# Kernel optimization log

Measured on AMD Instinct MI355X. Metric: run time of the kernel, lower is better.

The kernel has to match this reference:

```python
import jax, jax.numpy as jnp
import numpy as np

B, S, D, H, L = 4, 2048, 256, 4, 2
DK = D // H
V, T = 32000, 1000


def setup_inputs() -> dict:
    key = jax.random.key(0)
    ks = jax.random.split(key, 20)
    sc = 0.02
    event_emb = jax.random.normal(ks[0], (V, D), jnp.float32) * sc
    event_emb = event_emb.at[0].set(0.0)  # padding_idx=0
    time_emb = jax.random.normal(ks[1], (T, D), jnp.float32) * sc
    inp = {
        "x": jax.random.randint(ks[2], (B, S), 0, V, jnp.int32),
        "time_deltas": jax.random.randint(ks[3], (B, S), 0, T, jnp.int32),
        "mask": jax.random.randint(ks[4], (B, S), 0, 2, jnp.int32),
        "event_emb": event_emb,
        "time_emb": time_emb,
        "Wq": jax.random.normal(ks[5], (L, D, D), jnp.float32) * sc,
        "bq": jnp.zeros((L, D), jnp.float32),
        "Wk": jax.random.normal(ks[6], (L, D, D), jnp.float32) * sc,
        "bk": jnp.zeros((L, D), jnp.float32),
        "Wv": jax.random.normal(ks[7], (L, D, D), jnp.float32) * sc,
        "bv": jnp.zeros((L, D), jnp.float32),
        "time_proj": jax.random.normal(ks[8], (L, T, H), jnp.float32) * sc,
        "Wo": jax.random.normal(ks[9], (L, D, D), jnp.float32) * sc,
        "bo": jnp.zeros((L, D), jnp.float32),
        "ln_g": jnp.ones((L, D), jnp.float32),
        "ln_b": jnp.zeros((L, D), jnp.float32),
        "Wc1": jax.random.normal(ks[10], (D, D // 2), jnp.float32) * sc,
        "bc1": jnp.zeros((D // 2,), jnp.float32),
        "Wc2": jax.random.normal(ks[11], (D // 2, 1), jnp.float32) * sc,
        "bc2": jnp.zeros((1,), jnp.float32),
    }
    return inp


def _layernorm(h, g, b, eps=1e-5):
    mu = jnp.mean(h, -1, keepdims=True)
    var = jnp.mean(jnp.square(h - mu), -1, keepdims=True)
    return (h - mu) * jax.lax.rsqrt(var + eps) * g + b


def _attn(h, t_bins, mask, Wq, bq, Wk, bk, Wv, bv, tp, Wo, bo):
    b, s, d = h.shape
    q = (h @ Wq + bq).reshape(b, s, H, DK)
    k = (h @ Wk + bk).reshape(b, s, H, DK)
    v = (h @ Wv + bv).reshape(b, s, H, DK)
    scores = jnp.einsum("bqhd,bkhd->bhqk", q, k) / np.sqrt(DK).astype(np.float32)
    time_bias = tp[t_bins]  # [b,s,H] -> bias per key position
    scores = scores + jnp.transpose(time_bias, (0, 2, 1))[:, :, None, :]
    scores = jnp.where(mask[:, None, None, :] == 0, -1e9, scores)
    attn = jax.nn.softmax(scores, axis=-1)
    ctx = jnp.einsum("bhqk,bkhd->bqhd", attn, v).reshape(b, s, d)
    return ctx @ Wo + bo


def reference(x, time_deltas, mask, event_emb, time_emb, Wq, bq, Wk, bk, Wv, bv,
              time_proj, Wo, bo, ln_g, ln_b, Wc1, bc1, Wc2, bc2):
    t_bins = jnp.clip(time_deltas, 0, T - 1)
    h = event_emb[x] + time_emb[t_bins]
    for l in range(L):
        h = _attn(h, t_bins, mask, Wq[l], bq[l], Wk[l], bk[l], Wv[l], bv[l],
                  time_proj[l], Wo[l], bo[l])
        h = _layernorm(h, ln_g[l], ln_b[l])
    last = h[:, -1, :]
    hid = jax.nn.relu(last @ Wc1 + bc1)
    return jax.nn.sigmoid(hid @ Wc2 + bc2)
```

## Files before the change

### kernel.cpp

```cpp
#include <hip/hip_runtime.h>
#include <math.h>

namespace {

constexpr int NB = 4, NS = 2048, ND = 256, NH = 4, NDK = 64, NL = 2, NT = 1000;
constexpr float L2E = 1.44269504089f;
constexpr float QSCALE = 0.125f * L2E;

typedef short bfx8 __attribute__((ext_vector_type(8)));
typedef float f32x4 __attribute__((ext_vector_type(4)));

static __device__ __forceinline__ short f2bf(float f) {
  union { float f; unsigned u; } v; v.f = f;
  unsigned u = v.u;
  unsigned r = (u + 0x7fffu + ((u >> 16) & 1u)) >> 16;
  return (short)r;
}
static __device__ __forceinline__ float bf2f(short s) {
  union { float f; unsigned u; } v; v.u = ((unsigned)(unsigned short)s) << 16;
  return v.f;
}
static __device__ __forceinline__ float exp2_hw(float x) {
  float r;
  asm("v_exp_f32 %0, %1" : "=v"(r) : "v"(x));
  return r;
}
static __device__ __forceinline__ unsigned cvt_pk_bf16(float lo, float hi) {
  unsigned d;
  asm("v_cvt_pk_bf16_f32 %0, %1, %2" : "=v"(d) : "v"(lo), "v"(hi));
  return d;
}

__global__ __launch_bounds__(256) void k_packw(const float* __restrict__ Wq,
                                               const float* __restrict__ Wk,
                                               const float* __restrict__ Wv,
                                               const float* __restrict__ Wo,
                                               const float* __restrict__ bq,
                                               const float* __restrict__ bk,
                                               const float* __restrict__ bv,
                                               short* __restrict__ wqkvT,
                                               short* __restrict__ woT,
                                               float* __restrict__ bqkv) {
  __shared__ float t[64][65];
  int z = blockIdx.z, l = z >> 2, mat = z & 3;
  const float* src;
  short* dst;
  float scale = 1.f;
  if (mat == 0)      { src = Wq + (size_t)l * 65536; dst = wqkvT + (size_t)l * 768 * 256; scale = QSCALE; }
  else if (mat == 1) { src = Wk + (size_t)l * 65536; dst = wqkvT + (size_t)l * 768 * 256 + 256 * 256; }
  else if (mat == 2) { src = Wv + (size_t)l * 65536; dst = wqkvT + (size_t)l * 768 * 256 + 512 * 256; }
  else               { src = Wo + (size_t)l * 65536; dst = woT + (size_t)l * 65536; }
  int k0 = blockIdx.x * 64, n0 = blockIdx.y * 64;
  int c = threadIdx.x & 63, r4 = threadIdx.x >> 6;
  #pragma unroll
  for (int rr = 0; rr < 64; rr += 4) t[rr + r4][c] = src[(size_t)(k0 + rr + r4) * 256 + n0 + c];
  __syncthreads();
  #pragma unroll
  for (int rr = 0; rr < 64; rr += 4) {
    int n = rr + r4;
    dst[(size_t)(n0 + n) * 256 + k0 + c] = f2bf(t[c][n] * scale);
  }
  if (mat == 0 && blockIdx.x == 0 && blockIdx.y == 0) {
    for (int cc = threadIdx.x; cc < 768; cc += 256) {
      float v = cc < 256 ? bq[l * 256 + cc] * QSCALE
                         : (cc < 512 ? bk[l * 256 + cc - 256] : bv[l * 256 + cc - 512]);
      bqkv[l * 768 + cc] = v;
    }
  }
}

__global__ __launch_bounds__(256) void k_embed(const int* __restrict__ x,
                                               const int* __restrict__ td,
                                               const float* __restrict__ ee,
                                               const float* __restrict__ te,
                                               float* __restrict__ h,
                                               short* __restrict__ hb) {
  int lane = threadIdx.x & 63, r4 = threadIdx.x >> 6;
  int row = blockIdx.x * 4 + r4;
  int xi = x[row];
  int tb = td[row];
  tb = tb < 0 ? 0 : (tb >= NT ? NT - 1 : tb);
  float4 e = ((const float4*)&ee[(size_t)xi * ND])[lane];
  float4 tv = ((const float4*)&te[(size_t)tb * ND])[lane];
  float4 v;
  v.x = e.x + tv.x; v.y = e.y + tv.y; v.z = e.z + tv.z; v.w = e.w + tv.w;
  ((float4*)&h[(size_t)row * ND])[lane] = v;
  short4 ob; ob.x = f2bf(v.x); ob.y = f2bf(v.y); ob.z = f2bf(v.z); ob.w = f2bf(v.w);
  ((short4*)&hb[(size_t)row * ND])[lane] = ob;
}

template <int OUT_BF16>
__global__ __launch_bounds__(256) void k_gemm(const short* __restrict__ A,
                                              const short* __restrict__ BT,
                                              const float* __restrict__ bias,
                                              void* __restrict__ C, int ldc,
                                              int mb_mul, int mb_add, int n_base) {
  constexpr int LP = 76;
  __shared__ short at[64][LP];
  __shared__ short bt[128][LP];
  int tid = threadIdx.x;
  int w = tid >> 6, lane = tid & 63, ln15 = lane & 15, g = lane >> 4;
  int m0 = (blockIdx.x * mb_mul + mb_add) * 64;
  int n0 = n_base + blockIdx.y * 128;
  int srow = tid >> 2, scol = (tid & 3) * 16;
  int brow = tid >> 1, bcol = (tid & 1) * 32;

  f32x4 acc[8];
  #pragma unroll
  for (int nt = 0; nt < 8; ++nt) acc[nt] = (f32x4){0.f, 0.f, 0.f, 0.f};

  bfx8 a0, a1, b0, b1, b2, b3;
  auto LOAD = [&](int kk0) {
    const short* as = &A[(size_t)(m0 + srow) * 256 + kk0 + scol];
    a0 = *(const bfx8*)as; a1 = *(const bfx8*)(as + 8);
    const short* bs = &BT[(size_t)(n0 + brow) * 256 + kk0 + bcol];
    b0 = *(const bfx8*)bs; b1 = *(const bfx8*)(bs + 8);
    b2 = *(const bfx8*)(bs + 16); b3 = *(const bfx8*)(bs + 24);
  };
  LOAD(0);
  for (int kk0 = 0; kk0 < 256; kk0 += 64) {
    __syncthreads();
    *(bfx8*)&at[srow][scol] = a0; *(bfx8*)&at[srow][scol + 8] = a1;
    *(bfx8*)&bt[brow][bcol] = b0; *(bfx8*)&bt[brow][bcol + 8] = b1;
    *(bfx8*)&bt[brow][bcol + 16] = b2; *(bfx8*)&bt[brow][bcol + 24] = b3;
    __syncthreads();
    if (kk0 + 64 < 256) LOAD(kk0 + 64);
    #pragma unroll
    for (int ks = 0; ks < 2; ++ks) {
      bfx8 af = *(const bfx8*)&at[w * 16 + ln15][ks * 32 + g * 8];
      #pragma unroll
      for (int nt = 0; nt < 8; ++nt) {
        bfx8 bf = *(const bfx8*)&bt[nt * 16 + ln15][ks * 32 + g * 8];
        acc[nt] = __builtin_amdgcn_mfma_f32_16x16x32_bf16(af, bf, acc[nt], 0, 0, 0);
      }
    }
  }

  #pragma unroll
  for (int nt = 0; nt < 8; ++nt) {
    int col = n0 + nt * 16 + ln15;
    float bb = bias[col];
    #pragma unroll
    for (int r = 0; r < 4; ++r) {
      int row = m0 + w * 16 + g * 4 + r;
      float val = acc[nt][r] + bb;
      if (OUT_BF16) ((short*)C)[(size_t)row * ldc + col] = f2bf(val);
      else          ((float*)C)[(size_t)row * ldc + col] = val;
    }
  }
}

__global__ __launch_bounds__(256) void k_frag(const short* __restrict__ qkv,
                                              const int* __restrict__ td,
                                              const int* __restrict__ mask,
                                              const float* __restrict__ tp,
                                              short* __restrict__ vT,
                                              float* __restrict__ sbias_g) {
  __shared__ short vl[64][72];
  int tile = blockIdx.x, hh = blockIdx.y, b = blockIdx.z;
  int t = threadIdx.x;
  int k0 = tile * 64;
  {
    int key = t >> 2, dg = (t & 3) * 16;
    const short* vsrc = &qkv[(size_t)(b * NS + k0 + key) * 768 + 512 + hh * NDK + dg];
    bfx8 v0 = *(const bfx8*)vsrc, v1 = *(const bfx8*)(vsrc + 8);
    *(bfx8*)&vl[key][dg] = v0;
    *(bfx8*)&vl[key][dg + 8] = v1;
  }
  if (t < 64) {
    int kk = k0 + t;
    int tb = td[b * NS + kk];
    tb = tb < 0 ? 0 : (tb >= NT ? NT - 1 : tb);
    sbias_g[(size_t)(b * NH + hh) * NS + kk] = mask[b * NS + kk] ? tp[tb * NH + hh] * L2E : -1e9f;
  }
  __syncthreads();
  int dim = t >> 2, c0 = (t & 3) * 16;
  short outv[16];
  #pragma unroll
  for (int j = 0; j < 16; ++j) {
    int c = c0 + j;
    int kk = ((c >> 5) << 5) | (((c >> 2) & 1) << 4) | (((c >> 3) & 3) << 2) | (c & 3);
    outv[j] = vl[kk][dim];
  }
  short* dst = &vT[(((size_t)(b * NH + hh) * 32 + tile) * 64 + dim) * 64 + c0];
  *(int4*)dst = *(const int4*)outv;
  *(int4*)(dst + 8) = *(const int4*)(outv + 8);
}

__global__ __launch_bounds__(512, 4) void k_attn(const short* __restrict__ qkv,
                                                 const short* __restrict__ vT,
                                                 const float* __restrict__ sbias_g,
                                                 short* __restrict__ ctx,
                                                 short* __restrict__ partO,
                                                 float* __restrict__ partML,
                                                 int q_base, int qcount, int nchunk) {
  constexpr int LPK = 76;
  constexpr int LPV = 76;
  __shared__ short kt[2][64][LPK];
  __shared__ short vt[2][64][LPV];
  __shared__ float sbias[2][64];
  __shared__ float shML[128];

  int tid = threadIdx.x;
  int w = tid >> 6, lane = tid & 63, ln15 = lane & 15, g = lane >> 4;
  int half = w >> 2, wsub = w & 3;
  int t = tid & 255;
  int b = blockIdx.z, hh = blockIdx.y;
  int qtile = blockIdx.x / nchunk;
  int chunk = blockIdx.x - qtile * nchunk;
  int niter = NS / (128 * nchunk);
  int tbase = chunk * (NS / 64 / nchunk);
  int q0 = q_base + qtile * 64;
  int qw0 = q0 + wsub * 16;

  bfx8 aq[2];
  #pragma unroll
  for (int ks = 0; ks < 2; ++ks)
    aq[ks] = *(const bfx8*)&qkv[(size_t)(b * NS + qw0 + ln15) * 768 + hh * NDK + ks * 32 + g * 8];

  f32x4 o[4];
  #pragma unroll
  for (int dt = 0; dt < 4; ++dt) o[dt] = (f32x4){0.f, 0.f, 0.f, 0.f};
  float m = -1e30f, lsum = 0.f;

  int srow = t >> 2, scg = (t & 3) * 16;

  bfx8 kr0, kr1, vr0, vr1;
  float br = 0.f;
  auto loadset = [&](int it) {
    int tt = tbase + half * niter + it;
    int k0 = tt * 64;
    const short* ksrc = &qkv[(size_t)(b * NS + k0 + srow) * 768 + 256 + hh * NDK + scg];
    kr0 = *(const bfx8*)ksrc; kr1 = *(const bfx8*)(ksrc + 8);
    const short* vsrc = &vT[(((size_t)(b * NH + hh) * 32 + tt) * 64 + srow) * 64 + scg];
    vr0 = *(const bfx8*)vsrc; vr1 = *(const bfx8*)(vsrc + 8);
    if (t < 64) br = sbias_g[(size_t)(b * NH + hh) * NS + k0 + t];
  };

  auto compute = [&]() {
    f32x4 c[4];
    __builtin_amdgcn_s_setprio(1);
    #pragma unroll
    for (int nt = 0; nt < 4; ++nt) {
      c[nt] = (f32x4){0.f, 0.f, 0.f, 0.f};
      #pragma unroll
      for (int ks = 0; ks < 2; ++ks) {
        bfx8 kf = *(const bfx8*)&kt[half][nt * 16 + ln15][ks * 32 + g * 8];
        c[nt] = __builtin_amdgcn_mfma_f32_16x16x32_bf16(kf, aq[ks], c[nt], 0, 0, 0);
      }
    }
    __builtin_amdgcn_s_setprio(0);
    #pragma unroll
    for (int nt = 0; nt < 4; ++nt) {
      float4 bb = *(const float4*)&sbias[half][nt * 16 + g * 4];
      c[nt][0] += bb.x; c[nt][1] += bb.y; c[nt][2] += bb.z; c[nt][3] += bb.w;
    }
    float rm = c[0][0];
    #pragma unroll
    for (int nt = 0; nt < 4; ++nt)
      #pragma unroll
      for (int r = 0; r < 4; ++r) rm = fmaxf(rm, c[nt][r]);
    rm = fmaxf(rm, __shfl_xor(rm, 16, 64));
    rm = fmaxf(rm, __shfl_xor(rm, 32, 64));
    if (__any(rm > m + 10.f)) {
      float nm = fmaxf(m, rm);
      float scl = exp2_hw(m - nm);
      m = nm;
      lsum *= scl;
      #pragma unroll
      for (int dt = 0; dt < 4; ++dt)
        #pragma unroll
        for (int r = 0; r < 4; ++r) o[dt][r] *= scl;
    }
    unsigned pb[2][4];
    float ts = 0.f;
    #pragma unroll
    for (int nt = 0; nt < 4; ++nt) {
      float e0 = exp2_hw(c[nt][0] - m), e1 = exp2_hw(c[nt][1] - m);
      float e2 = exp2_hw(c[nt][2] - m), e3 = exp2_hw(c[nt][3] - m);
      ts += (e0 + e1) + (e2 + e3);
      pb[nt >> 1][(nt & 1) * 2]     = cvt_pk_bf16(e0, e1);
      pb[nt >> 1][(nt & 1) * 2 + 1] = cvt_pk_bf16(e2, e3);
    }
    lsum += ts;
    __builtin_amdgcn_s_setprio(1);
    #pragma unroll
    for (int ks = 0; ks < 2; ++ks) {
      union { unsigned u[4]; bfx8 v; } pf;
      pf.u[0] = pb[ks][0]; pf.u[1] = pb[ks][1]; pf.u[2] = pb[ks][2]; pf.u[3] = pb[ks][3];
      #pragma unroll
      for (int dt = 0; dt < 4; ++dt) {
        bfx8 vf = *(const bfx8*)&vt[half][dt * 16 + ln15][ks * 32 + g * 8];
        o[dt] = __builtin_amdgcn_mfma_f32_16x16x32_bf16(vf, pf.v, o[dt], 0, 0, 0);
      }
    }
    __builtin_amdgcn_s_setprio(0);
  };

  loadset(0);
  for (int it = 0; it < niter; ++it) {
    __syncthreads();
    *(bfx8*)&kt[half][srow][scg] = kr0;
    *(bfx8*)&kt[half][srow][scg + 8] = kr1;
    *(bfx8*)&vt[half][srow][scg] = vr0;
    *(bfx8*)&vt[half][srow][scg + 8] = vr1;
    if (t < 64) sbias[half][t] = br;
    __syncthreads();
    if (it + 1 < niter) loadset(it + 1);
    compute();
  }

  lsum += __shfl_xor(lsum, 16, 64);
  lsum += __shfl_xor(lsum, 32, 64);

  float* shO = (float*)&kt[0][0][0];
  __syncthreads();
  int q = wsub * 16 + ln15;
  if (half == 1) {
    #pragma unroll
    for (int dt = 0; dt < 4; ++dt) {
      float4 st; st.x = o[dt][0]; st.y = o[dt][1]; st.z = o[dt][2]; st.w = o[dt][3];
      *(float4*)&shO[q * 68 + dt * 16 + g * 4] = st;
    }
    if (g == 0) { shML[q * 2] = m; shML[q * 2 + 1] = lsum; }
  }
  __syncthreads();
  if (half == 0) {
    float m2 = shML[q * 2], l2 = shML[q * 2 + 1];
    float M = fmaxf(m, m2);
    float fa = exp2_hw(m - M), fb = exp2_hw(m2 - M);
    if (nchunk == 1) {
      float inv = 1.f / (lsum * fa + l2 * fb);
      fa *= inv; fb *= inv;
      #pragma unroll
      for (int dt = 0; dt < 4; ++dt) {
        float4 sh = *(const float4*)&shO[q * 68 + dt * 16 + g * 4];
        float v0 = o[dt][0] * fa + sh.x * fb;
        float v1 = o[dt][1] * fa + sh.y * fb;
        float v2 = o[dt][2] * fa + sh.z * fb;
        float v3 = o[dt][3] * fa + sh.w * fb;
        int2 pk; pk.x = (int)cvt_pk_bf16(v0, v1); pk.y = (int)cvt_pk_bf16(v2, v3);
        *(int2*)&ctx[(size_t)(b * NS + q0 + q) * ND + hh * NDK + dt * 16 + g * 4] = pk;
      }
    } else {
      float L = lsum * fa + l2 * fb;
      size_t rowi = (size_t)(chunk * 16 + b * NH + hh) * qcount + qtile * 64 + q;
      #pragma unroll
      for (int dt = 0; dt < 4; ++dt) {
        float4 sh = *(const float4*)&shO[q * 68 + dt * 16 + g * 4];
        float v0 = o[dt][0] * fa + sh.x * fb;
        float v1 = o[dt][1] * fa + sh.y * fb;
        float v2 = o[dt][2] * fa + sh.z * fb;
        float v3 = o[dt][3] * fa + sh.w * fb;
        int2 pk; pk.x = (int)cvt_pk_bf16(v0, v1); pk.y = (int)cvt_pk_bf16(v2, v3);
        *(int2*)&partO[rowi * 64 + dt * 16 + g * 4] = pk;
      }
      if (g == 0) { partML[rowi * 2] = M; partML[rowi * 2 + 1] = L; }
    }
  }
}

__global__ __launch_bounds__(256) void k_amerge(const short* __restrict__ partO,
                                                const float* __restrict__ partML,
                                                short* __restrict__ ctx,
                                                int q_base, int qcount, int nchunk) {
  int b = blockIdx.z, hh = blockIdx.y;
  int qi = blockIdx.x * 64 + (threadIdx.x >> 2);
  int d0 = (threadIdx.x & 3) * 16;
  int bh = b * NH + hh;
  float M = -1e30f;
  for (int c = 0; c < nchunk; ++c)
    M = fmaxf(M, partML[((size_t)(c * 16 + bh) * qcount + qi) * 2]);
  float L = 0.f;
  float acc[16];
  #pragma unroll
  for (int i = 0; i < 16; ++i) acc[i] = 0.f;
  for (int c = 0; c < nchunk; ++c) {
    size_t row = (size_t)(c * 16 + bh) * qcount + qi;
    float mc = partML[row * 2];
    float lc = partML[row * 2 + 1];
    float s = exp2_hw(mc - M);
    L += lc * s;
    union { int4 v; short sh[8]; } u0, u1;
    u0.v = *(const int4*)&partO[row * 64 + d0];
    u1.v = *(const int4*)&partO[row * 64 + d0 + 8];
    #pragma unroll
    for (int i = 0; i < 8; ++i) {
      acc[i]     += bf2f(u0.sh[i]) * s;
      acc[8 + i] += bf2f(u1.sh[i]) * s;
    }
  }
  float inv = 1.f / L;
  short res[16];
  #pragma unroll
  for (int i = 0; i < 16; ++i) res[i] = f2bf(acc[i] * inv);
  short* dst = &ctx[(size_t)(b * NS + q_base + qi) * ND + hh * NDK + d0];
  *(int4*)dst = *(const int4*)res;
  *(int4*)(dst + 8) = *(const int4*)(res + 8);
}

__global__ __launch_bounds__(256) void k_ln(float* __restrict__ h,
                                            short* __restrict__ hb,
                                            const float* __restrict__ g_,
                                            const float* __restrict__ b_, int q_base) {
  int lane = threadIdx.x & 63, r4 = threadIdx.x >> 6;
  size_t row = (size_t)blockIdx.y * NS + q_base + blockIdx.x * 4 + r4;
  float4 v = ((const float4*)&h[row * ND])[lane];
  float s = v.x + v.y + v.z + v.w;
  #pragma unroll
  for (int off = 1; off < 64; off <<= 1) s += __shfl_xor(s, off, 64);
  float mu = s * (1.f / ND);
  float dx = v.x - mu, dy = v.y - mu, dz = v.z - mu, dw = v.w - mu;
  float q = dx * dx + dy * dy + dz * dz + dw * dw;
  #pragma unroll
  for (int off = 1; off < 64; off <<= 1) q += __shfl_xor(q, off, 64);
  float rr = rsqrtf(q * (1.f / ND) + 1e-5f);
  float4 gg = ((const float4*)g_)[lane];
  float4 bb = ((const float4*)b_)[lane];
  float4 o;
  o.x = dx * rr * gg.x + bb.x;
  o.y = dy * rr * gg.y + bb.y;
  o.z = dz * rr * gg.z + bb.z;
  o.w = dw * rr * gg.w + bb.w;
  ((float4*)&h[row * ND])[lane] = o;
  short4 ob; ob.x = f2bf(o.x); ob.y = f2bf(o.y); ob.z = f2bf(o.z); ob.w = f2bf(o.w);
  ((short4*)&hb[row * ND])[lane] = ob;
}

__global__ __launch_bounds__(128) void k_head(const float* __restrict__ h,
                                              const float* __restrict__ Wc1,
                                              const float* __restrict__ bc1,
                                              const float* __restrict__ Wc2,
                                              const float* __restrict__ bc2,
                                              float* __restrict__ out) {
  __shared__ float red[128];
  int j = threadIdx.x;
  int b = blockIdx.x;
  const float* last = &h[(size_t)(b * NS + NS - 1) * ND];
  float acc = bc1[j];
  for (int d = 0; d < ND; ++d) acc = fmaf(last[d], Wc1[d * 128 + j], acc);
  acc = fmaxf(acc, 0.f);
  red[j] = acc * Wc2[j];
  __syncthreads();
  for (int off = 64; off > 0; off >>= 1) {
    if (j < off) red[j] += red[j + off];
    __syncthreads();
  }
  if (j == 0) out[b] = 1.f / (1.f + __expf(-(red[0] + bc2[0])));
}

}

extern "C" void kernel_launch(void* const* d_in, const int* in_sizes, int n_in,
                              void* d_out, int out_size, void* d_ws, size_t ws_size,
                              hipStream_t stream) {
  const int* x = (const int*)d_in[0];
  const int* td = (const int*)d_in[1];
  const int* mask = (const int*)d_in[2];
  const float* ee = (const float*)d_in[3];
  const float* te = (const float*)d_in[4];
  const float* Wq = (const float*)d_in[5];
  const float* bq = (const float*)d_in[6];
  const float* Wk = (const float*)d_in[7];
  const float* bk = (const float*)d_in[8];
  const float* Wv = (const float*)d_in[9];
  const float* bv = (const float*)d_in[10];
  const float* tp = (const float*)d_in[11];
  const float* Wo = (const float*)d_in[12];
  const float* bo = (const float*)d_in[13];
  const float* lng = (const float*)d_in[14];
  const float* lnb = (const float*)d_in[15];
  const float* Wc1 = (const float*)d_in[16];
  const float* bc1 = (const float*)d_in[17];
  const float* Wc2 = (const float*)d_in[18];
  const float* bc2 = (const float*)d_in[19];
  float* out = (float*)d_out;

  char* ws = (char*)d_ws;
  const size_t M = (size_t)NB * NS;
  float* h       = (float*)(ws);
  short* hb      = (short*)(ws + (8 << 20));
  short* qkv     = (short*)(ws + (12 << 20));
  short* ctx     = (short*)(ws + (24 << 20));
  short* wqkvT   = (short*)(ws + (28 << 20));
  short* woT     = (short*)(ws + (28 << 20) + 786432);
  float* bqkv    = (float*)(ws + (29 << 20) + 262144);
  short* vT      = (short*)(ws + (30 << 20));
  float* sbias_g = (float*)(ws + (34 << 20));
  short* partO   = (short*)(ws);
  float* partML  = (float*)(ws + (10 << 20));

  k_packw<<<dim3(4, 4, 8), 256, 0, stream>>>(Wq, Wk, Wv, Wo, bq, bk, bv, wqkvT, woT, bqkv);
  k_embed<<<NB * NS / 4, 256, 0, stream>>>(x, td, ee, te, h, hb);

  for (int l = 0; l < NL; ++l) {
    const short* wqkvTl = wqkvT + (size_t)l * 768 * 256;
    const short* woTl = woT + (size_t)l * 65536;
    const float* bqkvl = bqkv + (size_t)l * 768;
    const float* bol = bo + (size_t)l * ND;
    const float* tpl = tp + (size_t)l * NT * NH;
    const float* lngl = lng + (size_t)l * ND;
    const float* lnbl = lnb + (size_t)l * ND;
    const bool last = (l == NL - 1);

    if (!last) {
      k_gemm<1><<<dim3(M / 64, 6), 256, 0, stream>>>(hb, wqkvTl, bqkvl, qkv, 768, 1, 0, 0);
    } else {
      k_gemm<1><<<dim3(M / 64, 4), 256, 0, stream>>>(hb, wqkvTl, bqkvl, qkv, 768, 1, 0, 256);
      k_gemm<1><<<dim3(NB, 2), 256, 0, stream>>>(hb, wqkvTl, bqkvl, qkv, 768, 32, 31, 0);
    }

    k_frag<<<dim3(32, NH, NB), 256, 0, stream>>>(qkv, td, mask, tpl, vT, sbias_g);

    if (!last) {
      k_attn<<<dim3((NS / 64) * 2, NH, NB), 512, 0, stream>>>(qkv, vT, sbias_g, ctx,
                                                              partO, partML, 0, NS, 2);
      k_amerge<<<dim3(NS / 64, NH, NB), 256, 0, stream>>>(partO, partML, ctx, 0, NS, 2);
      k_gemm<0><<<dim3(M / 64, 2), 256, 0, stream>>>(ctx, woTl, bol, h, 256, 1, 0, 0);
      k_ln<<<dim3(NS / 4, NB), 256, 0, stream>>>(h, hb, lngl, lnbl, 0);
    } else {
      k_attn<<<dim3(16, NH, NB), 512, 0, stream>>>(qkv, vT, sbias_g, ctx,
                                                   partO, partML, NS - 64, 64, 16);
      k_amerge<<<dim3(1, NH, NB), 256, 0, stream>>>(partO, partML, ctx, NS - 64, 64, 16);
      k_gemm<0><<<dim3(NB, 2), 256, 0, stream>>>(ctx, woTl, bol, h, 256, 32, 31, 0);
      k_ln<<<dim3(1, NB), 256, 0, stream>>>(h, hb, lngl, lnbl, NS - 4);
    }
  }

  k_head<<<NB, 128, 0, stream>>>(h, Wc1, bc1, Wc2, bc2, out);
}
```

Baseline: 130.5 us.

## Process two 16-row query tiles per wave in attention to reuse K/V fragments

Each wave in the attention kernel now handles 32 query rows instead of 16, so every K and V fragment read from shared memory feeds two MFMAs. The block's query tile doubles to 128 and the grid halves. The last layer now computes 128 tail queries instead of 64. This cuts LDS traffic and loop overhead per unit of work, but roughly doubles accumulator registers, lowers the occupancy hint from 4 to 2, and halves the number of blocks, which may underfill the GPU.

```diff
diff --git a/kernel.cpp b/kernel.cpp
--- a/kernel.cpp
+++ b/kernel.cpp
@@ -187,19 +187,19 @@
   *(int4*)(dst + 8) = *(const int4*)(outv + 8);
 }
 
-__global__ __launch_bounds__(512, 4) void k_attn(const short* __restrict__ qkv,
+__global__ __launch_bounds__(512, 2) void k_attn(const short* __restrict__ qkv,
                                                  const short* __restrict__ vT,
                                                  const float* __restrict__ sbias_g,
                                                  short* __restrict__ ctx,
                                                  short* __restrict__ partO,
                                                  float* __restrict__ partML,
                                                  int q_base, int qcount, int nchunk) {
-  constexpr int LPK = 76;
-  constexpr int LPV = 76;
-  __shared__ short kt[2][64][LPK];
-  __shared__ short vt[2][64][LPV];
+  constexpr int LP = 76;
+  __shared__ short smem[2 * 2 * 64 * LP];
   __shared__ float sbias[2][64];
-  __shared__ float shML[128];
+  __shared__ float shML[256];
+  short (*kt)[64][LP] = (short(*)[64][LP])smem;
+  short (*vt)[64][LP] = (short(*)[64][LP])(smem + 2 * 64 * LP);
 
   int tid = threadIdx.x;
   int w = tid >> 6, lane = tid & 63, ln15 = lane & 15, g = lane >> 4;
@@ -210,18 +210,20 @@
   int chunk = blockIdx.x - qtile * nchunk;
   int niter = NS / (128 * nchunk);
   int tbase = chunk * (NS / 64 / nchunk);
-  int q0 = q_base + qtile * 64;
-  int qw0 = q0 + wsub * 16;
-
-  bfx8 aq[2];
-  #pragma unroll
-  for (int ks = 0; ks < 2; ++ks)
-    aq[ks] = *(const bfx8*)&qkv[(size_t)(b * NS + qw0 + ln15) * 768 + hh * NDK + ks * 32 + g * 8];
-
-  f32x4 o[4];
-  #pragma unroll
-  for (int dt = 0; dt < 4; ++dt) o[dt] = (f32x4){0.f, 0.f, 0.f, 0.f};
-  float m = -1e30f, lsum = 0.f;
+  int q0 = q_base + qtile * 128;
+  int qw0 = q0 + wsub * 32;
+
+  bfx8 aq0[2], aq1[2];
+  #pragma unroll
+  for (int ks = 0; ks < 2; ++ks) {
+    aq0[ks] = *(const bfx8*)&qkv[(size_t)(b * NS + qw0 + ln15) * 768 + hh * NDK + ks * 32 + g * 8];
+    aq1[ks] = *(const bfx8*)&qkv[(size_t)(b * NS + qw0 + 16 + ln15) * 768 + hh * NDK + ks * 32 + g * 8];
+  }
+
+  f32x4 o0[4], o1[4];
+  #pragma unroll
+  for (int dt = 0; dt < 4; ++dt) { o0[dt] = (f32x4){0.f,0.f,0.f,0.f}; o1[dt] = (f32x4){0.f,0.f,0.f,0.f}; }
+  float m0v = -1e30f, m1v = -1e30f, ls0 = 0.f, ls1 = 0.f;
 
   int srow = t >> 2, scg = (t & 3) * 16;
 
@@ -238,60 +240,69 @@
   };
 
   auto compute = [&]() {
-    f32x4 c[4];
+    f32x4 c0[4], c1[4];
     __builtin_amdgcn_s_setprio(1);
     #pragma unroll
     for (int nt = 0; nt < 4; ++nt) {
-      c[nt] = (f32x4){0.f, 0.f, 0.f, 0.f};
+      c0[nt] = (f32x4){0.f,0.f,0.f,0.f};
+      c1[nt] = (f32x4){0.f,0.f,0.f,0.f};
       #pragma unroll
       for (int ks = 0; ks < 2; ++ks) {
         bfx8 kf = *(const bfx8*)&kt[half][nt * 16 + ln15][ks * 32 + g * 8];
-        c[nt] = __builtin_amdgcn_mfma_f32_16x16x32_bf16(kf, aq[ks], c[nt], 0, 0, 0);
+        c0[nt] = __builtin_amdgcn_mfma_f32_16x16x32_bf16(kf, aq0[ks], c0[nt], 0, 0, 0);
+        c1[nt] = __builtin_amdgcn_mfma_f32_16x16x32_bf16(kf, aq1[ks], c1[nt], 0, 0, 0);
       }
     }
     __builtin_amdgcn_s_setprio(0);
     #pragma unroll
     for (int nt = 0; nt < 4; ++nt) {
       float4 bb = *(const float4*)&sbias[half][nt * 16 + g * 4];
-      c[nt][0] += bb.x; c[nt][1] += bb.y; c[nt][2] += bb.z; c[nt][3] += bb.w;
-    }
-    float rm = c[0][0];
+      c0[nt][0] += bb.x; c0[nt][1] += bb.y; c0[nt][2] += bb.z; c0[nt][3] += bb.w;
+      c1[nt][0] += bb.x; c1[nt][1] += bb.y; c1[nt][2] += bb.z; c1[nt][3] += bb.w;
+    }
+    float rm0 = c0[0][0], rm1 = c1[0][0];
     #pragma unroll
     for (int nt = 0; nt < 4; ++nt)
       #pragma unroll
-      for (int r = 0; r < 4; ++r) rm = fmaxf(rm, c[nt][r]);
-    rm = fmaxf(rm, __shfl_xor(rm, 16, 64));
-    rm = fmaxf(rm, __shfl_xor(rm, 32, 64));
-    if (__any(rm > m + 10.f)) {
-      float nm = fmaxf(m, rm);
-      float scl = exp2_hw(m - nm);
-      m = nm;
-      lsum *= scl;
+      for (int r = 0; r < 4; ++r) { rm0 = fmaxf(rm0, c0[nt][r]); rm1 = fmaxf(rm1, c1[nt][r]); }
+    rm0 = fmaxf(rm0, __shfl_xor(rm0, 16, 64)); rm0 = fmaxf(rm0, __shfl_xor(rm0, 32, 64));
+    rm1 = fmaxf(rm1, __shfl_xor(rm1, 16, 64)); rm1 = fmaxf(rm1, __shfl_xor(rm1, 32, 64));
+    if (__any((rm0 > m0v + 10.f) || (rm1 > m1v + 10.f))) {
+      float nm0 = fmaxf(m0v, rm0), nm1 = fmaxf(m1v, rm1);
+      float s0 = exp2_hw(m0v - nm0), s1 = exp2_hw(m1v - nm1);
+      m0v = nm0; m1v = nm1; ls0 *= s0; ls1 *= s1;
       #pragma unroll
       for (int dt = 0; dt < 4; ++dt)
         #pragma unroll
-        for (int r = 0; r < 4; ++r) o[dt][r] *= scl;
-    }
-    unsigned pb[2][4];
-    float ts = 0.f;
+        for (int r = 0; r < 4; ++r) { o0[dt][r] *= s0; o1[dt][r] *= s1; }
+    }
+    unsigned pb0[2][4], pb1[2][4];
+    float ts0 = 0.f, ts1 = 0.f;
     #pragma unroll
     for (int nt = 0; nt < 4; ++nt) {
-      float e0 = exp2_hw(c[nt][0] - m), e1 = exp2_hw(c[nt][1] - m);
-      float e2 = exp2_hw(c[nt][2] - m), e3 = exp2_hw(c[nt][3] - m);
-      ts += (e0 + e1) + (e2 + e3);
-      pb[nt >> 1][(nt & 1) * 2]     = cvt_pk_bf16(e0, e1);
-      pb[nt >> 1][(nt & 1) * 2 + 1] = cvt_pk_bf16(e2, e3);
-    }
-    lsum += ts;
+      float a0 = exp2_hw(c0[nt][0] - m0v), a1 = exp2_hw(c0[nt][1] - m0v);
+      float a2 = exp2_hw(c0[nt][2] - m0v), a3 = exp2_hw(c0[nt][3] - m0v);
+      ts0 += (a0 + a1) + (a2 + a3);
+      pb0[nt >> 1][(nt & 1) * 2]     = cvt_pk_bf16(a0, a1);
+      pb0[nt >> 1][(nt & 1) * 2 + 1] = cvt_pk_bf16(a2, a3);
+      float e0 = exp2_hw(c1[nt][0] - m1v), e1 = exp2_hw(c1[nt][1] - m1v);
+      float e2 = exp2_hw(c1[nt][2] - m1v), e3 = exp2_hw(c1[nt][3] - m1v);
+      ts1 += (e0 + e1) + (e2 + e3);
+      pb1[nt >> 1][(nt & 1) * 2]     = cvt_pk_bf16(e0, e1);
+      pb1[nt >> 1][(nt & 1) * 2 + 1] = cvt_pk_bf16(e2, e3);
+    }
+    ls0 += ts0; ls1 += ts1;
     __builtin_amdgcn_s_setprio(1);
     #pragma unroll
     for (int ks = 0; ks < 2; ++ks) {
-      union { unsigned u[4]; bfx8 v; } pf;
-      pf.u[0] = pb[ks][0]; pf.u[1] = pb[ks][1]; pf.u[2] = pb[ks][2]; pf.u[3] = pb[ks][3];
+      union { unsigned u[4]; bfx8 v; } pf0, pf1;
+      pf0.u[0] = pb0[ks][0]; pf0.u[1] = pb0[ks][1]; pf0.u[2] = pb0[ks][2]; pf0.u[3] = pb0[ks][3];
+      pf1.u[0] = pb1[ks][0]; pf1.u[1] = pb1[ks][1]; pf1.u[2] = pb1[ks][2]; pf1.u[3] = pb1[ks][3];
       #pragma unroll
       for (int dt = 0; dt < 4; ++dt) {
         bfx8 vf = *(const bfx8*)&vt[half][dt * 16 + ln15][ks * 32 + g * 8];
-        o[dt] = __builtin_amdgcn_mfma_f32_16x16x32_bf16(vf, pf.v, o[dt], 0, 0, 0);
+        o0[dt] = __builtin_amdgcn_mfma_f32_16x16x32_bf16(vf, pf0.v, o0[dt], 0, 0, 0);
+        o1[dt] = __builtin_amdgcn_mfma_f32_16x16x32_bf16(vf, pf1.v, o1[dt], 0, 0, 0);
       }
     }
     __builtin_amdgcn_s_setprio(0);
@@ -310,52 +321,64 @@
     compute();
   }
 
-  lsum += __shfl_xor(lsum, 16, 64);
-  lsum += __shfl_xor(lsum, 32, 64);
-
-  float* shO = (float*)&kt[0][0][0];
+  ls0 += __shfl_xor(ls0, 16, 64); ls0 += __shfl_xor(ls0, 32, 64);
+  ls1 += __shfl_xor(ls1, 16, 64); ls1 += __shfl_xor(ls1, 32, 64);
+
+  float* shO = (float*)smem;
   __syncthreads();
-  int q = wsub * 16 + ln15;
+  int qA = wsub * 32 + ln15, qB = qA + 16;
   if (half == 1) {
     #pragma unroll
     for (int dt = 0; dt < 4; ++dt) {
-      float4 st; st.x = o[dt][0]; st.y = o[dt][1]; st.z = o[dt][2]; st.w = o[dt][3];
-      *(float4*)&shO[q * 68 + dt * 16 + g * 4] = st;
-    }
-    if (g == 0) { shML[q * 2] = m; shML[q * 2 + 1] = lsum; }
+      float4 s0; s0.x = o0[dt][0]; s0.y = o0[dt][1]; s0.z = o0[dt][2]; s0.w = o0[dt][3];
+      *(float4*)&shO[qA * 68 + dt * 16 + g * 4] = s0;
+      float4 s1; s1.x = o1[dt][0]; s1.y = o1[dt][1]; s1.z = o1[dt][2]; s1.w = o1[dt][3];
+      *(float4*)&shO[qB * 68 + dt * 16 + g * 4] = s1;
+    }
+    if (g == 0) {
+      shML[qA * 2] = m0v; shML[qA * 2 + 1] = ls0;
+      shML[qB * 2] = m1v; shML[qB * 2 + 1] = ls1;
+    }
   }
   __syncthreads();
   if (half == 0) {
-    float m2 = shML[q * 2], l2 = shML[q * 2 + 1];
-    float M = fmaxf(m, m2);
-    float fa = exp2_hw(m - M), fb = exp2_hw(m2 - M);
-    if (nchunk == 1) {
-      float inv = 1.f / (lsum * fa + l2 * fb);
-      fa *= inv; fb *= inv;
-      #pragma unroll
-      for (int dt = 0; dt < 4; ++dt) {
-        float4 sh = *(const float4*)&shO[q * 68 + dt * 16 + g * 4];
-        float v0 = o[dt][0] * fa + sh.x * fb;
-        float v1 = o[dt][1] * fa + sh.y * fb;
-        float v2 = o[dt][2] * fa + sh.z * fb;
-        float v3 = o[dt][3] * fa + sh.w * fb;
-        int2 pk; pk.x = (int)cvt_pk_bf16(v0, v1); pk.y = (int)cvt_pk_bf16(v2, v3);
-        *(int2*)&ctx[(size_t)(b * NS + q0 + q) * ND + hh * NDK + dt * 16 + g * 4] = pk;
+    #pragma unroll
+    for (int qs = 0; qs < 2; ++qs) {
+      int q = qs ? qB : qA;
+      float mm = qs ? m1v : m0v;
+      float ll = qs ? ls1 : ls0;
+      const f32x4* oo = qs ? o1 : o0;
+      float m2 = shML[q * 2], l2 = shML[q * 2 + 1];
+      float M = fmaxf(mm, m2);
+      float fa = exp2_hw(mm - M), fb = exp2_hw(m2 - M);
+      if (nchunk == 1) {
+        float inv = 1.f / (ll * fa + l2 * fb);
+        fa *= inv; fb *= inv;
+        #pragma unroll
+        for (int dt = 0; dt < 4; ++dt) {
+          float4 sh = *(const float4*)&shO[q * 68 + dt * 16 + g * 4];
+          float v0 = oo[dt][0] * fa + sh.x * fb;
+          float v1 = oo[dt][1] * fa + sh.y * fb;
+          float v2 = oo[dt][2] * fa + sh.z * fb;
+          float v3 = oo[dt][3] * fa + sh.w * fb;
+          int2 pk; pk.x = (int)cvt_pk_bf16(v0, v1); pk.y = (int)cvt_pk_bf16(v2, v3);
+          *(int2*)&ctx[(size_t)(b * NS + q0 + q) * ND + hh * NDK + dt * 16 + g * 4] = pk;
+        }
+      } else {
+        float L = ll * fa + l2 * fb;
+        size_t rowi = (size_t)(chunk * 16 + b * NH + hh) * qcount + qtile * 128 + q;
+        #pragma unroll
+        for (int dt = 0; dt < 4; ++dt) {
+          float4 sh = *(const float4*)&shO[q * 68 + dt * 16 + g * 4];
+          float v0 = oo[dt][0] * fa + sh.x * fb;
+          float v1 = oo[dt][1] * fa + sh.y * fb;
+          float v2 = oo[dt][2] * fa + sh.z * fb;
+          float v3 = oo[dt][3] * fa + sh.w * fb;
+          int2 pk; pk.x = (int)cvt_pk_bf16(v0, v1); pk.y = (int)cvt_pk_bf16(v2, v3);
+          *(int2*)&partO[rowi * 64 + dt * 16 + g * 4] = pk;
+        }
+        if (g == 0) { partML[rowi * 2] = M; partML[rowi * 2 + 1] = L; }
       }
-    } else {
-      float L = lsum * fa + l2 * fb;
-      size_t rowi = (size_t)(chunk * 16 + b * NH + hh) * qcount + qtile * 64 + q;
-      #pragma unroll
-      for (int dt = 0; dt < 4; ++dt) {
-        float4 sh = *(const float4*)&shO[q * 68 + dt * 16 + g * 4];
-        float v0 = o[dt][0] * fa + sh.x * fb;
-        float v1 = o[dt][1] * fa + sh.y * fb;
-        float v2 = o[dt][2] * fa + sh.z * fb;
-        float v3 = o[dt][3] * fa + sh.w * fb;
-        int2 pk; pk.x = (int)cvt_pk_bf16(v0, v1); pk.y = (int)cvt_pk_bf16(v2, v3);
-        *(int2*)&partO[rowi * 64 + dt * 16 + g * 4] = pk;
-      }
-      if (g == 0) { partML[rowi * 2] = M; partML[rowi * 2 + 1] = L; }
     }
   }
 }
@@ -513,15 +536,15 @@
     k_frag<<<dim3(32, NH, NB), 256, 0, stream>>>(qkv, td, mask, tpl, vT, sbias_g);
 
     if (!last) {
-      k_attn<<<dim3((NS / 64) * 2, NH, NB), 512, 0, stream>>>(qkv, vT, sbias_g, ctx,
-                                                              partO, partML, 0, NS, 2);
+      k_attn<<<dim3((NS / 128) * 2, NH, NB), 512, 0, stream>>>(qkv, vT, sbias_g, ctx,
+                                                               partO, partML, 0, NS, 2);
       k_amerge<<<dim3(NS / 64, NH, NB), 256, 0, stream>>>(partO, partML, ctx, 0, NS, 2);
       k_gemm<0><<<dim3(M / 64, 2), 256, 0, stream>>>(ctx, woTl, bol, h, 256, 1, 0, 0);
       k_ln<<<dim3(NS / 4, NB), 256, 0, stream>>>(h, hb, lngl, lnbl, 0);
     } else {
       k_attn<<<dim3(16, NH, NB), 512, 0, stream>>>(qkv, vT, sbias_g, ctx,
-                                                   partO, partML, NS - 64, 64, 16);
-      k_amerge<<<dim3(1, NH, NB), 256, 0, stream>>>(partO, partML, ctx, NS - 64, 64, 16);
+                                                   partO, partML, NS - 128, 128, 16);
+      k_amerge<<<dim3(2, NH, NB), 256, 0, stream>>>(partO, partML, ctx, NS - 128, 128, 16);
       k_gemm<0><<<dim3(NB, 2), 256, 0, stream>>>(ctx, woTl, bol, h, 256, 32, 31, 0);
       k_ln<<<dim3(1, NB), 256, 0, stream>>>(h, hb, lngl, lnbl, NS - 4);
     }
```

Result: slower. 187.1 us (+43.4%).
